# Kernel optimization log

Hardware: AMD Instinct MI355X
Metric: run time of the kernel (lower is better)

Reference implementation:

```python
import jax, jax.numpy as jnp
import numpy as np

NUM_GRAPHS = 64  # number of graphs in the batch (static for segment reductions)


def gcn_conv(x, row, col, ew, W, b, N):
    """PyG GCNConv: x@W, symmetric gcn_norm with self-loops (weight 1), scatter-add, +bias."""
    xw = x @ W  # [N, F_out]
    # degree includes self-loop weight of 1.0 per node
    deg = jnp.zeros((N,), x.dtype).at[col].add(ew) + 1.0
    dis = jnp.where(deg > 0, jax.lax.rsqrt(deg), 0.0)  # deg^{-1/2}, inf -> 0
    norm = dis[row] * ew * dis[col]  # [E]
    agg = jnp.zeros_like(xw).at[col].add(xw[row] * norm[:, None])
    agg = agg + xw * (dis * dis)[:, None]  # self-loop contribution: 1/deg
    return agg + b


def global_mean_pool(x, batch, num_graphs):
    s = jnp.zeros((num_graphs, x.shape[1]), x.dtype).at[batch].add(x)
    cnt = jnp.zeros((num_graphs,), x.dtype).at[batch].add(1.0)
    return s / jnp.maximum(cnt, 1.0)[:, None]


def setup_inputs() -> dict:
    key = jax.random.key(0)
    ks = jax.random.split(key, 10)
    N, E, C_in, C_hid, C_out = 40000, 640000, 128, 128, 64
    flat = 6 * 22 * 22  # num_time_intervals * (2*num_nodes)^2 = 2904
    x = jax.random.normal(ks[0], (N, C_in), jnp.float32)
    edge_index = jax.random.randint(ks[1], (2, E), 0, N, jnp.int64)
    edge_weight = jax.random.uniform(ks[2], (E,), jnp.float32)
    batch = jnp.sort(jax.random.randint(ks[3], (N,), 0, NUM_GRAPHS, jnp.int64))
    W1 = jax.random.normal(ks[4], (C_in, C_hid), jnp.float32) / np.sqrt(C_in)
    b1 = jnp.zeros((C_hid,), jnp.float32)
    W2 = jax.random.normal(ks[5], (C_hid, C_out), jnp.float32) / np.sqrt(C_hid)
    b2 = jnp.zeros((C_out,), jnp.float32)
    Wfc = jax.random.normal(ks[6], (C_out, flat), jnp.float32) / np.sqrt(C_out)
    bfc = jnp.zeros((flat,), jnp.float32)
    return {"x": x, "edge_index": edge_index, "edge_weight": edge_weight, "batch": batch,
            "W1": W1, "b1": b1, "W2": W2, "b2": b2, "Wfc": Wfc, "bfc": bfc}


def reference(x, edge_index, edge_weight, batch, W1, b1, W2, b2, Wfc, bfc):
    N = x.shape[0]
    row, col = edge_index[0], edge_index[1]
    h = jax.nn.relu(gcn_conv(x, row, col, edge_weight, W1, b1, N))
    h = jax.nn.relu(gcn_conv(h, row, col, edge_weight, W2, b2, N))
    g = global_mean_pool(h, batch, NUM_GRAPHS)  # [G, C_out]
    return g @ Wfc + bfc  # [G, 2904] predicted flattened adjacency
```

## Files before the change

### kernel.cpp

```cpp
#include <hip/hip_runtime.h>
#include <hip/hip_bf16.h>
#include <hip/hip_fp16.h>
#include <type_traits>

#define NG 64
#define FLAT 2904
#define K128 128
#define BKB 256

typedef _Float16 h4 __attribute__((ext_vector_type(4)));
typedef _Float16 half8 __attribute__((ext_vector_type(8)));
typedef float f32x4 __attribute__((ext_vector_type(4)));

__device__ __forceinline__ float4 ld4(const float* p) { return *(const float4*)p; }
__device__ __forceinline__ float4 ldh4(const _Float16* p) {
    h4 h = *(const h4*)p;
    return make_float4((float)h.x, (float)h.y, (float)h.z, (float)h.w);
}
__device__ __forceinline__ void sth4(_Float16* p, float4 v) {
    h4 h; h.x = (_Float16)v.x; h.y = (_Float16)v.y; h.z = (_Float16)v.z; h.w = (_Float16)v.w;
    *(h4*)p = h;
}
__device__ __forceinline__ float unpack_w(unsigned q) {
    return (float)__builtin_bit_cast(_Float16, (unsigned short)(q & 0xFFFFu));
}

__global__ __launch_bounds__(256) void k_init(int* __restrict__ bhist,
                                              int* __restrict__ bcursor,
                                              float* __restrict__ g,
                                              int* __restrict__ gcnt,
                                              const float* __restrict__ W1,
                                              const float* __restrict__ W2,
                                              _Float16* __restrict__ Wt1,
                                              _Float16* __restrict__ Wt2) {
    int tid = threadIdx.x;
    if (blockIdx.x == 0) {
        bhist[tid] = 0; bcursor[tid] = 0;
        for (int i = tid; i < NG * 64; i += 256) g[i] = 0.f;
        if (tid < NG) gcnt[tid] = 0;
    }
    int idx = blockIdx.x * 256 + tid;
    if (idx < 128 * 128) {
        int n = idx % 128, k = idx / 128;
        Wt1[n * K128 + k] = (_Float16)W1[k * 128 + n];
    } else if (idx < 128 * 128 + 64 * 128) {
        int i = idx - 128 * 128;
        int n = i % 64, k = i / 64;
        Wt2[n * K128 + k] = (_Float16)W2[k * 64 + n];
    }
}


__global__ __launch_bounds__(256) void k_bhist(const int* __restrict__ col,
                                               int* __restrict__ bhist, int E, int nbk) {
    __shared__ int h[BKB];
    int tid = threadIdx.x;
    for (int i = tid; i < nbk; i += 256) h[i] = 0;
    __syncthreads();
    int base = blockIdx.x * 1024 + tid * 4;
#pragma unroll
    for (int q = 0; q < 4; q++) {
        int e = base + q;
        if (e < E) atomicAdd(&h[col[e] >> 8], 1);
    }
    __syncthreads();
    for (int i = tid; i < nbk; i += 256) if (h[i]) atomicAdd(&bhist[i], h[i]);
}

__global__ __launch_bounds__(256) void k_bucket(const int* __restrict__ row,
                                                const int* __restrict__ col,
                                                const float* __restrict__ ew,
                                                const int* __restrict__ bhist,
                                                int* __restrict__ bcursor,
                                                uint2* __restrict__ bk, int E, int nbk) {
    __shared__ int part[256];
    __shared__ int h[BKB];
    __shared__ int cur[BKB];
    int tid = threadIdx.x;
    int gh = (tid < nbk) ? bhist[tid] : 0;
    part[tid] = gh;
    h[tid] = 0;
    __syncthreads();
    for (int off = 1; off < 256; off <<= 1) {
        int t = (tid >= off) ? part[tid - off] : 0;
        __syncthreads();
        part[tid] += t;
        __syncthreads();
    }
    int ex = part[tid] - gh;
    int base = blockIdx.x * 1024 + tid * 4;
    int c[4];
#pragma unroll
    for (int q = 0; q < 4; q++) {
        int e = base + q;
        c[q] = (e < E) ? col[e] : -1;
        if (c[q] >= 0) atomicAdd(&h[c[q] >> 8], 1);
    }
    __syncthreads();
    if (tid < nbk) cur[tid] = h[tid] ? ex + atomicAdd(&bcursor[tid], h[tid]) : 0;
    __syncthreads();
#pragma unroll
    for (int q = 0; q < 4; q++) {
        int e = base + q;
        if (c[q] >= 0) {
            int slot = atomicAdd(&cur[c[q] >> 8], 1);
            bk[slot] = make_uint2(((unsigned)c[q] << 16) | (unsigned)row[e],
                                  __float_as_uint(ew[e]));
        }
    }
}

__global__ __launch_bounds__(256) void k_colsedata(const uint2* __restrict__ bk,
                                                   const int* __restrict__ bhist,
                                                   float* __restrict__ dis,
                                                   int* __restrict__ rs,
                                                   unsigned* __restrict__ edata,
                                                   int N, int E, int nbk) {
    constexpr int CAP = 5120;
    __shared__ int part[256];
    __shared__ float sdeg[BKB];
    __shared__ int scnt[BKB];
    __shared__ int cur[BKB];
    __shared__ float sdis[BKB];
    __shared__ int sse[2];
    __shared__ uint2 ebuf[CAP];
    int b = blockIdx.x, tid = threadIdx.x;
    int gh = (tid < nbk) ? bhist[tid] : 0;
    part[tid] = gh;
    sdeg[tid] = 0.f; scnt[tid] = 0;
    __syncthreads();
    for (int off = 1; off < 256; off <<= 1) {
        int t = (tid >= off) ? part[tid - off] : 0;
        __syncthreads();
        part[tid] += t;
        __syncthreads();
    }
    if (tid == b) { sse[0] = part[tid] - gh; sse[1] = part[tid]; }
    __syncthreads();
    int s = sse[0], e = sse[1];
    int n = e - s;
    for (int i = tid; i < n; i += 256) {
        uint2 q = bk[s + i];
        if (i < CAP) ebuf[i] = q;
        int c8 = (q.x >> 16) & 255;
        atomicAdd(&sdeg[c8], __uint_as_float(q.y));
        atomicAdd(&scnt[c8], 1);
    }
    __syncthreads();
    int cnt = scnt[tid];
    part[tid] = cnt;
    __syncthreads();
    for (int off = 1; off < 256; off <<= 1) {
        int t = (tid >= off) ? part[tid - off] : 0;
        __syncthreads();
        part[tid] += t;
        __syncthreads();
    }
    float d  = rsqrtf(sdeg[tid] + 1.0f);
    int   r0 = s + part[tid] - cnt;
    int gcol = b * BKB + tid;
    if (gcol < N) { dis[gcol] = d; rs[gcol] = r0; }
    if (b == 0 && tid == 0) rs[N] = E;
    cur[tid] = r0; sdis[tid] = d;
    __syncthreads();
    for (int i = tid; i < n; i += 256) {
        uint2 q = (i < CAP) ? ebuf[i] : bk[s + i];
        int c8 = (q.x >> 16) & 255;
        unsigned r = q.x & 0xFFFFu;
        _Float16 wh = (_Float16)(__uint_as_float(q.y) * sdis[c8]);
        int pos = atomicAdd(&cur[c8], 1);
        edata[pos] = (r << 16) | (unsigned)__builtin_bit_cast(unsigned short, wh);
    }
}

__global__ __launch_bounds__(256) void k_gemm1(const float* __restrict__ A,
                                               const _Float16* __restrict__ Wt,
                                               const float* __restrict__ dis,
                                               _Float16* __restrict__ out, int M) {
    constexpr int NCOL = 128, AS = 136;
    __shared__ _Float16 Ah[64 * AS];
    __shared__ _Float16 Wh[NCOL * AS];

    int tid  = threadIdx.x;
    int row0 = blockIdx.x * 64;
#pragma unroll
    for (int q = 0; q < 8; q++) {
        int idx = tid + 256 * q;
        int r = idx >> 5, c4 = (idx & 31) * 4;
        float4 v = ld4(A + (size_t)(row0 + r) * K128 + c4);
        sth4(&Ah[r * AS + c4], v);
    }
#pragma unroll
    for (int q = 0; q < NCOL / 16; q++) {
        int idx = tid + 256 * q;
        int n = idx >> 4, c8 = (idx & 15) * 8;
        *(half8*)&Wh[n * AS + c8] = *(const half8*)(Wt + n * K128 + c8);
    }
    __syncthreads();

    int lane = tid & 63, wv = tid >> 6, m = lane & 15, quad = lane >> 4;
    f32x4 acc[NCOL / 16];
#pragma unroll
    for (int ct = 0; ct < NCOL / 16; ct++) acc[ct] = (f32x4){0.f, 0.f, 0.f, 0.f};
#pragma unroll
    for (int kt = 0; kt < 4; kt++) {
        half8 af = *(const half8*)&Ah[(wv * 16 + m) * AS + kt * 32 + quad * 8];
#pragma unroll
        for (int ct = 0; ct < NCOL / 16; ct++) {
            half8 bf = *(const half8*)&Wh[(ct * 16 + m) * AS + kt * 32 + quad * 8];
            acc[ct] = __builtin_amdgcn_mfma_f32_16x16x32_f16(af, bf, acc[ct], 0, 0, 0);
        }
    }
    float d[4];
#pragma unroll
    for (int r = 0; r < 4; r++) d[r] = dis[row0 + wv * 16 + quad * 4 + r];
#pragma unroll
    for (int ct = 0; ct < NCOL / 16; ct++)
#pragma unroll
        for (int r = 0; r < 4; r++) {
            int grow = row0 + wv * 16 + quad * 4 + r;
            out[(size_t)grow * NCOL + ct * 16 + m] = (_Float16)(acc[ct][r] * d[r]);
        }
}

__global__ __launch_bounds__(256) void k_agg_gemm(const _Float16* __restrict__ xw,
                                                  const float* __restrict__ dis,
                                                  const unsigned* __restrict__ edata,
                                                  const int* __restrict__ rs,
                                                  const float* __restrict__ bias,
                                                  const _Float16* __restrict__ Wt2,
                                                  _Float16* __restrict__ xw2, int N) {
    constexpr int F = 128, AS = 136;
    __shared__ _Float16 Hs[16 * AS];
    __shared__ _Float16 Ws[64 * AS];

    int tid   = threadIdx.x;
    int node0 = blockIdx.x * 16;
    int nl    = tid >> 4;
    int node  = node0 + nl;
    int j8    = (tid & 15) * 8;

#pragma unroll
    for (int q = 0; q < 4; q++) {
        int idx = tid + 256 * q;
        int n = idx >> 4, c8 = (idx & 15) * 8;
        *(half8*)&Ws[n * AS + c8] = *(const half8*)(Wt2 + n * K128 + c8);
    }

    float a0[8], a1[8], a2[8], a3[8];
    {
        float dv = dis[node];
        half8 sv = *(const half8*)(xw + (size_t)node * F + j8);
        float4 bA = ld4(bias + j8), bB = ld4(bias + j8 + 4);
#pragma unroll
        for (int t = 0; t < 4; t++) { a0[t] = (float)sv[t] * dv + (&bA.x)[t];
                                      a0[t + 4] = (float)sv[t + 4] * dv + (&bB.x)[t]; }
#pragma unroll
        for (int t = 0; t < 8; t++) { a1[t] = 0.f; a2[t] = 0.f; a3[t] = 0.f; }
    }
    int s = rs[node], e = rs[node + 1];
    int j = s;
    for (; j + 4 <= e; j += 4) {
        unsigned q0 = edata[j + 0], q1 = edata[j + 1], q2 = edata[j + 2], q3 = edata[j + 3];
        half8 v0 = *(const half8*)(xw + (size_t)(q0 >> 16) * F + j8);
        half8 v1 = *(const half8*)(xw + (size_t)(q1 >> 16) * F + j8);
        half8 v2 = *(const half8*)(xw + (size_t)(q2 >> 16) * F + j8);
        half8 v3 = *(const half8*)(xw + (size_t)(q3 >> 16) * F + j8);
        float n0 = unpack_w(q0), n1 = unpack_w(q1), n2 = unpack_w(q2), n3 = unpack_w(q3);
#pragma unroll
        for (int t = 0; t < 8; t++) {
            a0[t] += n0 * (float)v0[t];
            a1[t] += n1 * (float)v1[t];
            a2[t] += n2 * (float)v2[t];
            a3[t] += n3 * (float)v3[t];
        }
    }
    for (; j < e; j++) {
        unsigned q = edata[j];
        half8 v = *(const half8*)(xw + (size_t)(q >> 16) * F + j8);
        float nm = unpack_w(q);
#pragma unroll
        for (int t = 0; t < 8; t++) a0[t] += nm * (float)v[t];
    }
    half8 hv;
#pragma unroll
    for (int t = 0; t < 8; t++)
        hv[t] = (_Float16)fmaxf((a0[t] + a1[t]) + (a2[t] + a3[t]), 0.f);
    *(half8*)&Hs[nl * AS + j8] = hv;
    __syncthreads();

    int lane = tid & 63, wv = tid >> 6, m = lane & 15, quad = lane >> 4;
    f32x4 acc = (f32x4){0.f, 0.f, 0.f, 0.f};
#pragma unroll
    for (int kt = 0; kt < 4; kt++) {
        half8 af = *(const half8*)&Hs[m * AS + kt * 32 + quad * 8];
        half8 bf = *(const half8*)&Ws[(wv * 16 + m) * AS + kt * 32 + quad * 8];
        acc = __builtin_amdgcn_mfma_f32_16x16x32_f16(af, bf, acc, 0, 0, 0);
    }
#pragma unroll
    for (int r = 0; r < 4; r++) {
        int gn = node0 + quad * 4 + r;
        xw2[(size_t)gn * 64 + wv * 16 + m] = (_Float16)(acc[r] * dis[gn]);
    }
}

__global__ __launch_bounds__(256) void k_agg_pool(const _Float16* __restrict__ xw,
                                                  const float* __restrict__ dis,
                                                  const unsigned* __restrict__ edata,
                                                  const int* __restrict__ rs,
                                                  const float* __restrict__ bias,
                                                  const int* __restrict__ batch,
                                                  float* __restrict__ g,
                                                  int* __restrict__ gcnt, int N) {
    constexpr int F = 64;
    __shared__ float T[16][F + 4];
    __shared__ int sb[16];
    int tid  = threadIdx.x;
    int base = blockIdx.x * 16;
    int nl   = tid >> 4;
    int node = base + nl;
    int j4   = (tid & 15) * 4;
    if (tid < 16) sb[tid] = batch[base + tid];

    float dv = dis[node];
    float4 self = ldh4(xw + (size_t)node * F + j4);
    float4 bv   = ld4(bias + j4);
    float4 a0 = make_float4(self.x * dv + bv.x, self.y * dv + bv.y,
                            self.z * dv + bv.z, self.w * dv + bv.w);
    float4 a1 = make_float4(0.f, 0.f, 0.f, 0.f);
    float4 a2 = a1, a3 = a1;
    int s = rs[node], e = rs[node + 1];
    int j = s;
    for (; j + 4 <= e; j += 4) {
        unsigned q0 = edata[j + 0], q1 = edata[j + 1], q2 = edata[j + 2], q3 = edata[j + 3];
        float4 v0 = ldh4(xw + (size_t)(q0 >> 16) * F + j4);
        float4 v1 = ldh4(xw + (size_t)(q1 >> 16) * F + j4);
        float4 v2 = ldh4(xw + (size_t)(q2 >> 16) * F + j4);
        float4 v3 = ldh4(xw + (size_t)(q3 >> 16) * F + j4);
        float n0 = unpack_w(q0), n1 = unpack_w(q1), n2 = unpack_w(q2), n3 = unpack_w(q3);
        a0.x += n0 * v0.x; a0.y += n0 * v0.y; a0.z += n0 * v0.z; a0.w += n0 * v0.w;
        a1.x += n1 * v1.x; a1.y += n1 * v1.y; a1.z += n1 * v1.z; a1.w += n1 * v1.w;
        a2.x += n2 * v2.x; a2.y += n2 * v2.y; a2.z += n2 * v2.z; a2.w += n2 * v2.w;
        a3.x += n3 * v3.x; a3.y += n3 * v3.y; a3.z += n3 * v3.z; a3.w += n3 * v3.w;
    }
    for (; j < e; j++) {
        unsigned q = edata[j];
        float nm = unpack_w(q);
        float4 v = ldh4(xw + (size_t)(q >> 16) * F + j4);
        a0.x += nm * v.x; a0.y += nm * v.y; a0.z += nm * v.z; a0.w += nm * v.w;
    }
    T[nl][j4 + 0] = fmaxf((a0.x + a1.x) + (a2.x + a3.x), 0.f);
    T[nl][j4 + 1] = fmaxf((a0.y + a1.y) + (a2.y + a3.y), 0.f);
    T[nl][j4 + 2] = fmaxf((a0.z + a1.z) + (a2.z + a3.z), 0.f);
    T[nl][j4 + 3] = fmaxf((a0.w + a1.w) + (a2.w + a3.w), 0.f);
    __syncthreads();
    if (tid < 64) {
        int f = tid;
        float run = 0.f;
        int cur = -1, cnt = 0;
        for (int k = 0; k < 16; k++) {
            int b = sb[k];
            if (b != cur) {
                if (cur >= 0) {
                    atomicAdd(&g[cur * 64 + f], run);
                    if (f == 0) atomicAdd(&gcnt[cur], cnt);
                }
                cur = b; run = 0.f; cnt = 0;
            }
            run += T[k][f];
            cnt++;
        }
        atomicAdd(&g[cur * 64 + f], run);
        if (f == 0) atomicAdd(&gcnt[cur], cnt);
    }
}

__global__ __launch_bounds__(256) void k_fc(const float* __restrict__ g,
                                            const int* __restrict__ gcnt,
                                            const float* __restrict__ Wfc,
                                            const float* __restrict__ bfc,
                                            float* __restrict__ out) {
    __shared__ float gs[64];
    int i = blockIdx.y;
    int j = blockIdx.x * blockDim.x + threadIdx.x;
    if (threadIdx.x < 64) {
        float c = (float)gcnt[i];
        gs[threadIdx.x] = g[i * 64 + threadIdx.x] / fmaxf(c, 1.0f);
    }
    __syncthreads();
    if (j >= FLAT) return;
    float acc = bfc[j];
#pragma unroll 8
    for (int k = 0; k < 64; k++) acc += gs[k] * Wfc[k * FLAT + j];
    out[(size_t)i * FLAT + j] = acc;
}

extern "C" void kernel_launch(void* const* d_in, const int* in_sizes, int n_in,
                              void* d_out, int out_size, void* d_ws, size_t ws_size,
                              hipStream_t stream) {
    const float* x    = (const float*)d_in[0];
    const int*   ei   = (const int*)d_in[1];
    const float* ew   = (const float*)d_in[2];
    const int*   batch= (const int*)d_in[3];
    const float* W1   = (const float*)d_in[4];
    const float* b1   = (const float*)d_in[5];
    const float* W2   = (const float*)d_in[6];
    const float* b2   = (const float*)d_in[7];
    const float* Wfc  = (const float*)d_in[8];
    const float* bfc  = (const float*)d_in[9];
    float* out = (float*)d_out;

    const int N = in_sizes[0] / K128;
    const int E = in_sizes[2];
    const int* row = ei;
    const int* col = ei + E;
    const int nbk = (N + BKB - 1) / BKB;
    const int neb = (E + 1023) / 1024;

    char* p = (char*)d_ws;
    auto alloc = [&](size_t bytes) -> void* {
        void* r = (void*)p;
        p += (bytes + 255) & ~(size_t)255;
        return r;
    };
    float*     dis   = (float*)    alloc((size_t)N * 4);
    int*       rs    = (int*)      alloc((size_t)(N + 1) * 4);
    uint2*     bk    = (uint2*)    alloc((size_t)E * 8);
    unsigned*  edata = (unsigned*) alloc((size_t)E * 4);
    _Float16*  xw1   = (_Float16*) alloc((size_t)N * 128 * 2);
    _Float16*  xw2   = (_Float16*) alloc((size_t)N * 64 * 2);
    _Float16*  Wt1   = (_Float16*) alloc((size_t)128 * 128 * 2);
    _Float16*  Wt2   = (_Float16*) alloc((size_t)64 * 128 * 2);
    float*     g     = (float*)    alloc(64 * 64 * 4);
    int*       gcnt  = (int*)      alloc(64 * 4);
    int*       bhist = (int*)      alloc(BKB * 4);
    int*       bcur  = (int*)      alloc(BKB * 4);

    k_init     <<<96,  256, 0, stream>>>(bhist, bcur, g, gcnt, W1, W2, Wt1, Wt2);
    k_bhist    <<<neb, 256, 0, stream>>>(col, bhist, E, nbk);
    k_bucket   <<<neb, 256, 0, stream>>>(row, col, ew, bhist, bcur, bk, E, nbk);
    k_colsedata<<<nbk, 256, 0, stream>>>(bk, bhist, dis, rs, edata, N, E, nbk);

    k_gemm1    <<<N / 64, 256, 0, stream>>>(x, Wt1, dis, xw1, N);
    k_agg_gemm <<<N / 16, 256, 0, stream>>>(xw1, dis, edata, rs, b1, Wt2, xw2, N);
    k_agg_pool <<<N / 16, 256, 0, stream>>>(xw2, dis, edata, rs, b2, batch, g, gcnt, N);

    dim3 fcg((FLAT + 255) / 256, NG);
    k_fc<<<fcg, 256, 0, stream>>>(g, gcnt, Wfc, bfc, out);
}
```

Before: 192.8 us.

## Use wave-shuffle scans in column bucketing and widen pooled aggregation to 8 features per thread

```diff
diff --git a/kernel.cpp b/kernel.cpp
--- a/kernel.cpp
+++ b/kernel.cpp
@@ -117,52 +117,79 @@
                                                    unsigned* __restrict__ edata,
                                                    int N, int E, int nbk) {
     constexpr int CAP = 5120;
-    __shared__ int part[256];
     __shared__ float sdeg[BKB];
     __shared__ int scnt[BKB];
     __shared__ int cur[BKB];
     __shared__ float sdis[BKB];
+    __shared__ int wsum[4];
     __shared__ int sse[2];
     __shared__ uint2 ebuf[CAP];
     int b = blockIdx.x, tid = threadIdx.x;
+    int lane = tid & 63, wv = tid >> 6;
     int gh = (tid < nbk) ? bhist[tid] : 0;
-    part[tid] = gh;
     sdeg[tid] = 0.f; scnt[tid] = 0;
-    __syncthreads();
-    for (int off = 1; off < 256; off <<= 1) {
-        int t = (tid >= off) ? part[tid - off] : 0;
-        __syncthreads();
-        part[tid] += t;
-        __syncthreads();
-    }
-    if (tid == b) { sse[0] = part[tid] - gh; sse[1] = part[tid]; }
+
+    int v = gh;
+#pragma unroll
+    for (int off = 1; off < 64; off <<= 1) {
+        int t = __shfl_up(v, off);
+        if (lane >= off) v += t;
+    }
+    if (lane == 63) wsum[wv] = v;
+    __syncthreads();
+    if (wv > 0) {
+        int add = 0;
+        for (int k = 0; k < wv; k++) add += wsum[k];
+        v += add;
+    }
+    if (tid == b) { sse[0] = v - gh; sse[1] = v; }
     __syncthreads();
     int s = sse[0], e = sse[1];
     int n = e - s;
-    for (int i = tid; i < n; i += 256) {
-        uint2 q = bk[s + i];
-        if (i < CAP) ebuf[i] = q;
-        int c8 = (q.x >> 16) & 255;
-        atomicAdd(&sdeg[c8], __uint_as_float(q.y));
-        atomicAdd(&scnt[c8], 1);
-    }
-    __syncthreads();
+
+    for (int i0 = tid; i0 < n; i0 += 2048) {
+        uint2 q[8]; bool gv[8];
+#pragma unroll
+        for (int u = 0; u < 8; u++) {
+            int i = i0 + u * 256;
+            gv[u] = i < n;
+            if (gv[u]) q[u] = bk[s + i];
+        }
+#pragma unroll
+        for (int u = 0; u < 8; u++) {
+            if (gv[u]) {
+                int i = i0 + u * 256;
+                if (i < CAP) ebuf[i] = q[u];
+                int c8 = (q[u].x >> 16) & 255;
+                atomicAdd(&sdeg[c8], __uint_as_float(q[u].y));
+                atomicAdd(&scnt[c8], 1);
+            }
+        }
+    }
+    __syncthreads();
+
     int cnt = scnt[tid];
-    part[tid] = cnt;
-    __syncthreads();
-    for (int off = 1; off < 256; off <<= 1) {
-        int t = (tid >= off) ? part[tid - off] : 0;
-        __syncthreads();
-        part[tid] += t;
-        __syncthreads();
+    int v2 = cnt;
+#pragma unroll
+    for (int off = 1; off < 64; off <<= 1) {
+        int t = __shfl_up(v2, off);
+        if (lane >= off) v2 += t;
+    }
+    if (lane == 63) wsum[wv] = v2;
+    __syncthreads();
+    if (wv > 0) {
+        int add = 0;
+        for (int k = 0; k < wv; k++) add += wsum[k];
+        v2 += add;
     }
     float d  = rsqrtf(sdeg[tid] + 1.0f);
-    int   r0 = s + part[tid] - cnt;
+    int   r0 = s + v2 - cnt;
     int gcol = b * BKB + tid;
     if (gcol < N) { dis[gcol] = d; rs[gcol] = r0; }
     if (b == 0 && tid == 0) rs[N] = E;
     cur[tid] = r0; sdis[tid] = d;
     __syncthreads();
+
     for (int i = tid; i < n; i += 256) {
         uint2 q = (i < CAP) ? ebuf[i] : bk[s + i];
         int c8 = (q.x >> 16) & 255;
@@ -313,59 +340,64 @@
                                                   float* __restrict__ g,
                                                   int* __restrict__ gcnt, int N) {
     constexpr int F = 64;
-    __shared__ float T[16][F + 4];
-    __shared__ int sb[16];
+    __shared__ float T[32][F + 4];
+    __shared__ int sb[32];
     int tid  = threadIdx.x;
-    int base = blockIdx.x * 16;
-    int nl   = tid >> 4;
+    int base = blockIdx.x * 32;
+    int nl   = tid >> 3;
     int node = base + nl;
-    int j4   = (tid & 15) * 4;
-    if (tid < 16) sb[tid] = batch[base + tid];
+    int j8   = (tid & 7) * 8;
+    if (tid < 32) sb[tid] = batch[base + tid];
 
     float dv = dis[node];
-    float4 self = ldh4(xw + (size_t)node * F + j4);
-    float4 bv   = ld4(bias + j4);
-    float4 a0 = make_float4(self.x * dv + bv.x, self.y * dv + bv.y,
-                            self.z * dv + bv.z, self.w * dv + bv.w);
-    float4 a1 = make_float4(0.f, 0.f, 0.f, 0.f);
-    float4 a2 = a1, a3 = a1;
+    half8 sv = *(const half8*)(xw + (size_t)node * F + j8);
+    float4 bA = ld4(bias + j8), bB = ld4(bias + j8 + 4);
+    float a0[8], a1[8], a2[8], a3[8];
+#pragma unroll
+    for (int t = 0; t < 4; t++) { a0[t] = (float)sv[t] * dv + (&bA.x)[t];
+                                  a0[t + 4] = (float)sv[t + 4] * dv + (&bB.x)[t]; }
+#pragma unroll
+    for (int t = 0; t < 8; t++) { a1[t] = 0.f; a2[t] = 0.f; a3[t] = 0.f; }
     int s = rs[node], e = rs[node + 1];
     int j = s;
     for (; j + 4 <= e; j += 4) {
         unsigned q0 = edata[j + 0], q1 = edata[j + 1], q2 = edata[j + 2], q3 = edata[j + 3];
-        float4 v0 = ldh4(xw + (size_t)(q0 >> 16) * F + j4);
-        float4 v1 = ldh4(xw + (size_t)(q1 >> 16) * F + j4);
-        float4 v2 = ldh4(xw + (size_t)(q2 >> 16) * F + j4);
-        float4 v3 = ldh4(xw + (size_t)(q3 >> 16) * F + j4);
+        half8 v0 = *(const half8*)(xw + (size_t)(q0 >> 16) * F + j8);
+        half8 v1 = *(const half8*)(xw + (size_t)(q1 >> 16) * F + j8);
+        half8 v2 = *(const half8*)(xw + (size_t)(q2 >> 16) * F + j8);
+        half8 v3 = *(const half8*)(xw + (size_t)(q3 >> 16) * F + j8);
         float n0 = unpack_w(q0), n1 = unpack_w(q1), n2 = unpack_w(q2), n3 = unpack_w(q3);
-        a0.x += n0 * v0.x; a0.y += n0 * v0.y; a0.z += n0 * v0.z; a0.w += n0 * v0.w;
-        a1.x += n1 * v1.x; a1.y += n1 * v1.y; a1.z += n1 * v1.z; a1.w += n1 * v1.w;
-        a2.x += n2 * v2.x; a2.y += n2 * v2.y; a2.z += n2 * v2.z; a2.w += n2 * v2.w;
-        a3.x += n3 * v3.x; a3.y += n3 * v3.y; a3.z += n3 * v3.z; a3.w += n3 * v3.w;
+#pragma unroll
+        for (int t = 0; t < 8; t++) {
+            a0[t] += n0 * (float)v0[t];
+            a1[t] += n1 * (float)v1[t];
+            a2[t] += n2 * (float)v2[t];
+            a3[t] += n3 * (float)v3[t];
+        }
     }
     for (; j < e; j++) {
         unsigned q = edata[j];
+        half8 v = *(const half8*)(xw + (size_t)(q >> 16) * F + j8);
         float nm = unpack_w(q);
-        float4 v = ldh4(xw + (size_t)(q >> 16) * F + j4);
-        a0.x += nm * v.x; a0.y += nm * v.y; a0.z += nm * v.z; a0.w += nm * v.w;
-    }
-    T[nl][j4 + 0] = fmaxf((a0.x + a1.x) + (a2.x + a3.x), 0.f);
-    T[nl][j4 + 1] = fmaxf((a0.y + a1.y) + (a2.y + a3.y), 0.f);
-    T[nl][j4 + 2] = fmaxf((a0.z + a1.z) + (a2.z + a3.z), 0.f);
-    T[nl][j4 + 3] = fmaxf((a0.w + a1.w) + (a2.w + a3.w), 0.f);
+#pragma unroll
+        for (int t = 0; t < 8; t++) a0[t] += nm * (float)v[t];
+    }
+#pragma unroll
+    for (int t = 0; t < 8; t++)
+        T[nl][j8 + t] = fmaxf((a0[t] + a1[t]) + (a2[t] + a3[t]), 0.f);
     __syncthreads();
     if (tid < 64) {
         int f = tid;
         float run = 0.f;
         int cur = -1, cnt = 0;
-        for (int k = 0; k < 16; k++) {
-            int b = sb[k];
-            if (b != cur) {
+        for (int k = 0; k < 32; k++) {
+            int bb = sb[k];
+            if (bb != cur) {
                 if (cur >= 0) {
                     atomicAdd(&g[cur * 64 + f], run);
                     if (f == 0) atomicAdd(&gcnt[cur], cnt);
                 }
-                cur = b; run = 0.f; cnt = 0;
+                cur = bb; run = 0.f; cnt = 0;
             }
             run += T[k][f];
             cnt++;
@@ -443,7 +475,7 @@
 
     k_gemm1    <<<N / 64, 256, 0, stream>>>(x, Wt1, dis, xw1, N);
     k_agg_gemm <<<N / 16, 256, 0, stream>>>(xw1, dis, edata, rs, b1, Wt2, xw2, N);
-    k_agg_pool <<<N / 16, 256, 0, stream>>>(xw2, dis, edata, rs, b2, batch, g, gcnt, N);
+    k_agg_pool <<<N / 32, 256, 0, stream>>>(xw2, dis, edata, rs, b2, batch, g, gcnt, N);
 
     dim3 fcg((FLAT + 255) / 256, NG);
     k_fc<<<fcg, 256, 0, stream>>>(g, gcnt, Wfc, bfc, out);
```

Result: faster. 182.9 us (-5.1%).
